# Optimization experiments

Hardware: AMD Instinct MI355X
Metric: run time of the kernel (lower is better)

The kernel has to match this reference:

```python
import jax, jax.numpy as jnp
import numpy as np

B, LC, LQ, D, F = 16, 2048, 256, 768, 768
MASK_VALUE = -1.0e12


def setup_inputs() -> dict:
    key = jax.random.key(0)
    ks = jax.random.split(key, 6)
    scale = 1.0 / np.sqrt(D)
    return {
        "x_cont": jax.random.normal(ks[0], (B, LC, D), dtype=jnp.float32),
        "x_ques": jax.random.normal(ks[1], (B, LQ, D), dtype=jnp.float32),
        "ques_len": jax.random.randint(ks[2], (B, 1), 0, LQ, dtype=jnp.int32),
        "WC": jax.random.normal(ks[3], (D, F), dtype=jnp.float32) * scale,
        "WQ": jax.random.normal(ks[4], (D, F), dtype=jnp.float32) * scale,
        "V": jax.random.normal(ks[5], (2 * D, F), dtype=jnp.float32) * scale,
    }


def _mask_logits(logits, ques_len):
    # Original: one_hot(ques_len[:,0], Lq) -> 1 - cumsum along Lq -> tile over Lc.
    # mask[b, j] = 1 if j < ques_len[b] else 0.
    lq = logits.shape[-1]
    oh = jax.nn.one_hot(ques_len[:, 0], lq, dtype=jnp.float32)  # [B, Lq]
    valid = 1.0 - jnp.cumsum(oh, axis=1)                         # [B, Lq]
    return logits + MASK_VALUE * (1.0 - valid)[:, None, :]       # broadcast over Lc


def reference(x_cont, x_ques, ques_len, WC, WQ, V):
    filters = WC.shape[-1]
    x_cont_ = jax.nn.relu(jnp.einsum("bcd,df->bcf", x_cont, WC))  # [B, Lc, F]
    x_ques_ = jax.nn.relu(jnp.einsum("bqd,df->bqf", x_ques, WQ))  # [B, Lq, F]
    logits = jnp.einsum("bcf,bqf->bcq", x_cont_, x_ques_) / jnp.sqrt(
        jnp.asarray(filters, dtype=x_cont.dtype)
    )  # [B, Lc, Lq]
    logits = _mask_logits(logits, ques_len)
    attn = jax.nn.softmax(logits, axis=-1)
    C = jnp.einsum("bcq,bqd->bcd", attn, x_ques)                  # [B, Lc, D]
    res = jnp.concatenate([x_cont, C], axis=2)                    # [B, Lc, 2D]
    gate = jax.nn.sigmoid(jnp.einsum("bce,ef->bcf", res, V))      # [B, Lc, F]
    return gate
```

## Files before the change

kernel.cpp:

```cpp
#include <hip/hip_runtime.h>
#include <hip/hip_bf16.h>
#include <cstdint>


using bf16 = __hip_bfloat16;
typedef __attribute__((ext_vector_type(8))) __bf16 bf16x8;
typedef __attribute__((ext_vector_type(4))) float f32x4;

typedef __attribute__((address_space(1))) const uint32_t GU32;
typedef __attribute__((address_space(3))) uint32_t LU32;

__device__ __forceinline__ void gll16(const bf16* g, bf16* l) {
  __builtin_amdgcn_global_load_lds((GU32*)g, (LU32*)l, 16, 0, 0);
}
__device__ __forceinline__ f32x4 mfma_bf16(bf16x8 a, bf16x8 b, f32x4 c) {
  return __builtin_amdgcn_mfma_f32_16x16x32_bf16(a, b, c, 0, 0, 0);
}
__device__ __forceinline__ bf16x8 ld_frag(const bf16* p) {
  return *reinterpret_cast<const bf16x8*>(p);
}
__device__ __forceinline__ int swz(int r) { return (r & 3) ^ ((r >> 2) & 1); }

__device__ __forceinline__ unsigned short f2bf_bits(float x) {
  bf16 b = __float2bfloat16(x);
  union { bf16 b; unsigned short s; } u;
  u.b = b;
  return u.s;
}

__global__ __launch_bounds__(256) void prep(
    const float* __restrict__ WC, const float* __restrict__ WQ,
    const float* __restrict__ V, const float* __restrict__ x_cont,
    const float* __restrict__ x_ques,
    bf16* __restrict__ Wct, bf16* __restrict__ Wqt,
    bf16* __restrict__ xcB, bf16* __restrict__ xqB) {
  const int bid = blockIdx.x;
  const int tid = threadIdx.x;
  if (bid < 2304) {
    __shared__ float tile[32][33];
    const int z = bid / 576, t = bid % 576;
    const float* in = (z == 0) ? WC : (z == 1) ? WQ : (z == 2) ? V : V + (long)768 * 768;
    bf16* out = (z == 0) ? Wct : (z == 1) ? Wqt
              : (z == 2) ? Wct + (long)768 * 768 : Wqt + (long)768 * 768;
    const int c0 = (t % 24) * 32, r0 = (t / 24) * 32;
    const int tx = tid & 31, ty = tid >> 5;
#pragma unroll
    for (int i = ty; i < 32; i += 8)
      tile[i][tx] = in[(long)(r0 + i) * 768 + (c0 + tx)];
    __syncthreads();
#pragma unroll
    for (int i = ty; i < 32; i += 8)
      out[(long)(c0 + i) * 768 + (r0 + tx)] = __float2bfloat16(tile[tx][i]);
  } else if (bid < 5376) {
    long i = (long)(bid - 2304) * 256 + tid;
#pragma unroll
    for (int k = 0; k < 8; ++k, i += 786432) {
      float4 v = reinterpret_cast<const float4*>(x_cont)[i];
      ushort4 o;
      o.x = f2bf_bits(v.x); o.y = f2bf_bits(v.y);
      o.z = f2bf_bits(v.z); o.w = f2bf_bits(v.w);
      reinterpret_cast<ushort4*>(xcB)[i] = o;
    }
  } else {
    long i = (long)(bid - 5376) * 256 + tid;
#pragma unroll
    for (int k = 0; k < 4; ++k, i += 196608) {
      float4 v = reinterpret_cast<const float4*>(x_ques)[i];
      ushort4 o;
      o.x = f2bf_bits(v.x); o.y = f2bf_bits(v.y);
      o.z = f2bf_bits(v.z); o.w = f2bf_bits(v.w);
      reinterpret_cast<ushort4*>(xqB)[i] = o;
    }
  }
}

__global__ __launch_bounds__(256) void gemm_bt_split(
    const bf16* __restrict__ A, long lda,
    const bf16* __restrict__ Bt, long ldb,
    bf16* __restrict__ O1, bf16* __restrict__ O2t, int K) {
  __shared__ __align__(16) bf16 As[128 * 32];
  __shared__ __align__(16) bf16 Bs[128 * 32];
  const int tid = threadIdx.x;
  const int wave = tid >> 6;
  const int lane = tid & 63;
  const int l16 = lane & 15;
  const int kh = lane >> 4;
  const int wm = (wave >> 1) * 64;
  const int wn = (wave & 1) * 64;
  const long row0 = (long)blockIdx.x * 128;
  const long col0 = (long)blockIdx.y * 128;
  const int srow = tid >> 2;
  const int scol = ((tid & 3) ^ swz(srow)) * 8;

  const bf16* ap0 = A + (row0 + srow) * lda + scol;
  const bf16* ap1 = ap0 + 64 * lda;
  const bf16* bp0 = Bt + (col0 + srow) * ldb + scol;
  const bf16* bp1 = bp0 + 64 * ldb;
  bf16* as0 = As + wave * 512;
  bf16* as1 = as0 + 2048;
  bf16* bs0 = Bs + wave * 512;
  bf16* bs1 = bs0 + 2048;

  const int xc = (kh ^ swz(l16)) * 8;
  f32x4 acc[4][4] = {};

  for (int k0 = 0; k0 < K; k0 += 32) {
    gll16(ap0 + k0, as0);
    gll16(ap1 + k0, as1);
    gll16(bp0 + k0, bs0);
    gll16(bp1 + k0, bs1);
    __syncthreads();
    bf16x8 af[4], bfr[4];
#pragma unroll
    for (int i = 0; i < 4; ++i)
      af[i] = ld_frag(As + (wm + i * 16 + l16) * 32 + xc);
#pragma unroll
    for (int j = 0; j < 4; ++j)
      bfr[j] = ld_frag(Bs + (wn + j * 16 + l16) * 32 + xc);
#pragma unroll
    for (int i = 0; i < 4; ++i)
#pragma unroll
      for (int j = 0; j < 4; ++j)
        acc[i][j] = mfma_bf16(af[i], bfr[j], acc[i][j]);
    __syncthreads();
  }

  const bool isO1 = col0 < 768;
#pragma unroll
  for (int i = 0; i < 4; ++i)
#pragma unroll
    for (int j = 0; j < 4; ++j) {
      const long rowb = row0 + wm + i * 16 + kh * 4;
      const long col = col0 + wn + j * 16 + l16;
      if (isO1) {
#pragma unroll
        for (int r = 0; r < 4; ++r)
          O1[(rowb + r) * 768 + col] = __float2bfloat16(fmaxf(acc[i][j][r], 0.0f));
      } else {
        const int d = (int)(col - 768);
        const int b2 = (int)(rowb >> 8);
        const int q = (int)(rowb & 255);
        ushort4 u;
        u.x = f2bf_bits(acc[i][j][0]);
        u.y = f2bf_bits(acc[i][j][1]);
        u.z = f2bf_bits(acc[i][j][2]);
        u.w = f2bf_bits(acc[i][j][3]);
        *reinterpret_cast<ushort4*>(O2t + ((long)b2 * 768 + d) * 256 + q) = u;
      }
    }
}

__global__ __launch_bounds__(512, 2) void gemm4b(
    const bf16* __restrict__ A, long lda,
    const bf16* __restrict__ Bt, long ldb,
    bf16* __restrict__ O1, bf16* __restrict__ O2, int K) {
  extern __shared__ __align__(16) bf16 smem[];
  const int tid = threadIdx.x;
  const int wid = tid >> 6;
  const int lane = tid & 63;
  const int l15 = lane & 15;
  const int g = lane >> 4;
  const int wm = wid >> 2;
  const int wn = wid & 3;

  const int lin = blockIdx.x;
  const int per = (int)gridDim.x >> 3;
  const int wgid = (lin & 7) * per + (lin >> 3);
  const long row0 = (long)(wgid / 6) * 256;
  const long col0 = (long)(wgid % 6) * 256;

  const int srow = lane >> 2;
  const int sc = ((lane & 3) ^ swz(srow)) * 8;
  const int w16 = wid * 16;
  const bf16* Ab = A + (row0 + srow) * lda + sc;
  const bf16* Bb = Bt + (col0 + srow) * ldb + sc;

  f32x4 acc[8][4] = {};

  auto stageA = [&](int buf, int kk) {
    bf16* d = smem + buf * 16384 + w16 * 32;
    gll16(Ab + (long)w16 * lda + kk, d);
    gll16(Ab + (long)(128 + w16) * lda + kk, d + 128 * 32);
  };
  auto stageB = [&](int buf, int kk) {
    bf16* d = smem + buf * 16384 + 8192 + w16 * 32;
    gll16(Bb + (long)w16 * ldb + kk, d);
    gll16(Bb + (long)(128 + w16) * ldb + kk, d + 128 * 32);
  };
  const int xc = (g ^ swz(l15)) * 8;
  auto ldA = [&](int buf, int m) {
    int row = wm * 128 + m * 16 + l15;
    return ld_frag(smem + buf * 16384 + row * 32 + xc);
  };
  auto ldB = [&](int buf, int n) {
    int row = wn * 64 + n * 16 + l15;
    return ld_frag(smem + buf * 16384 + 8192 + row * 32 + xc);
  };

  stageA(0, 0);
  stageB(0, 0);
  stageA(1, 32);
  stageB(1, 32);
  stageA(2, 64);
  stageB(2, 64);

  const int NT = K >> 5;
  bf16x8 av[4], bv[4];

  for (int t = 0; t < NT; ++t) {
    const int cur = t & 3;

    if (t <= NT - 3)
      asm volatile("s_waitcnt vmcnt(8)\n\ts_barrier" ::: "memory");
    else if (t == NT - 2)
      asm volatile("s_waitcnt vmcnt(4)\n\ts_barrier" ::: "memory");
    else
      asm volatile("s_waitcnt vmcnt(0)\n\ts_barrier" ::: "memory");

    if (t + 3 < NT) {
      stageA((t + 3) & 3, (t + 3) << 5);
      stageB((t + 3) & 3, (t + 3) << 5);
    }

#pragma unroll
    for (int n = 0; n < 4; ++n) bv[n] = ldB(cur, n);
#pragma unroll
    for (int m = 0; m < 4; ++m) av[m] = ldA(cur, m);
    __builtin_amdgcn_s_setprio(1);
#pragma unroll
    for (int m = 0; m < 4; ++m)
#pragma unroll
      for (int n = 0; n < 4; ++n) acc[m][n] = mfma_bf16(av[m], bv[n], acc[m][n]);
    __builtin_amdgcn_s_setprio(0);

#pragma unroll
    for (int m = 0; m < 4; ++m) av[m] = ldA(cur, 4 + m);
    __builtin_amdgcn_s_setprio(1);
#pragma unroll
    for (int m = 0; m < 4; ++m)
#pragma unroll
      for (int n = 0; n < 4; ++n)
        acc[4 + m][n] = mfma_bf16(av[m], bv[n], acc[4 + m][n]);
    __builtin_amdgcn_s_setprio(0);
  }

  const bool isO1 = col0 < 768;
#pragma unroll
  for (int m = 0; m < 8; ++m)
#pragma unroll
    for (int n = 0; n < 4; ++n)
#pragma unroll
      for (int r = 0; r < 4; ++r) {
        long row = row0 + wm * 128 + m * 16 + g * 4 + r;
        long col = col0 + wn * 64 + n * 16 + l15;
        float v = acc[m][n][r];
        if (isO1)
          O1[row * 768 + col] = __float2bfloat16(fmaxf(v, 0.0f));
        else
          O2[row * 768 + (col - 768)] = __float2bfloat16(v);
      }
}

__global__ __launch_bounds__(512) void attn3(
    const bf16* __restrict__ xcW, const bf16* __restrict__ xqW,
    const bf16* __restrict__ xqVT, const bf16* __restrict__ G1,
    const int* __restrict__ qlen_arr, float* __restrict__ out) {
  extern __shared__ __align__(16) bf16 smem[];
  bf16* P = smem;
  float* wred = (float*)(smem + 49152);
  float* wsum = wred + 512;

  const int lin = blockIdx.x;
  const int xcd = lin & 7;
  const int jj = lin >> 3;
  const int b = xcd * 2 + (jj >> 4);
  const int ct = jj & 15;

  const int tid = threadIdx.x;
  const int wid = tid >> 6;
  const int lane = tid & 63;
  const int l16 = lane & 15;
  const int kh = lane >> 4;
  const int wm = wid >> 2;
  const int wn = wid & 3;

  const long crow0 = (long)b * 2048 + (long)ct * 128;
  const int srow = lane >> 2;
  const int sc = ((lane & 3) ^ swz(srow)) * 8;
  const int xcr = (kh ^ swz(l16)) * 8;

  const bf16* ap = xcW + (crow0 + wid * 16 + srow) * 768 + sc;
  const bf16* bp = xqW + ((long)b * 256 + wid * 32 + srow) * 768 + sc;
  const bf16* bp2 = bp + 16 * 768;

  auto stage = [&](int buf, int k0) {
    gll16(ap + k0, smem + buf * 12288 + wid * 512);
    bf16* bd = smem + buf * 12288 + 4096 + wid * 1024;
    gll16(bp + k0, bd);
    gll16(bp2 + k0, bd + 512);
  };

  f32x4 acc[4][4] = {};
  stage(0, 0);
  stage(1, 32);
  stage(2, 64);

  for (int t = 0; t < 24; ++t) {
    const int cur = t & 3;

    if (t <= 21)
      asm volatile("s_waitcnt vmcnt(6)\n\ts_barrier" ::: "memory");
    else if (t == 22)
      asm volatile("s_waitcnt vmcnt(3)\n\ts_barrier" ::: "memory");
    else
      asm volatile("s_waitcnt vmcnt(0)\n\ts_barrier" ::: "memory");

    if (t + 3 < 24) stage((t + 3) & 3, (t + 3) * 32);

    const bf16* Ac = smem + cur * 12288;
    const bf16* Bc = Ac + 4096;
    bf16x8 af[4], bfr[4];
#pragma unroll
    for (int i = 0; i < 4; ++i)
      af[i] = ld_frag(Ac + (wm * 64 + i * 16 + l16) * 32 + xcr);
#pragma unroll
    for (int j = 0; j < 4; ++j)
      bfr[j] = ld_frag(Bc + (wn * 64 + j * 16 + l16) * 32 + xcr);
    __builtin_amdgcn_s_setprio(1);
#pragma unroll
    for (int i = 0; i < 4; ++i)
#pragma unroll
      for (int j = 0; j < 4; ++j)
        acc[i][j] = mfma_bf16(af[i], bfr[j], acc[i][j]);
    __builtin_amdgcn_s_setprio(0);
  }

  const float scale = 0.036084391824351615f;
  const int qlen = qlen_arr[b];

#pragma unroll
  for (int i = 0; i < 4; ++i)
#pragma unroll
    for (int j = 0; j < 4; ++j) {
      int col = wn * 64 + j * 16 + l16;
      float m = (col >= qlen) ? -1.0e12f : 0.0f;
#pragma unroll
      for (int r = 0; r < 4; ++r)
        acc[i][j][r] = acc[i][j][r] * scale + m;
    }

#pragma unroll
  for (int i = 0; i < 4; ++i)
#pragma unroll
    for (int r = 0; r < 4; ++r) {
      float mx = fmaxf(fmaxf(acc[i][0][r], acc[i][1][r]),
                       fmaxf(acc[i][2][r], acc[i][3][r]));
      mx = fmaxf(mx, __shfl_xor(mx, 1));
      mx = fmaxf(mx, __shfl_xor(mx, 2));
      mx = fmaxf(mx, __shfl_xor(mx, 4));
      mx = fmaxf(mx, __shfl_xor(mx, 8));
      if (l16 == 0) wred[(wm * 64 + i * 16 + kh * 4 + r) * 4 + wn] = mx;
    }
  __syncthreads();

#pragma unroll
  for (int i = 0; i < 4; ++i)
#pragma unroll
    for (int r = 0; r < 4; ++r) {
      int row = wm * 64 + i * 16 + kh * 4 + r;
      float gm = fmaxf(fmaxf(wred[row * 4 + 0], wred[row * 4 + 1]),
                       fmaxf(wred[row * 4 + 2], wred[row * 4 + 3]));
      float s = 0.0f;
#pragma unroll
      for (int j = 0; j < 4; ++j) {
        float e = __expf(acc[i][j][r] - gm);
        acc[i][j][r] = e;
        s += e;
      }
      s += __shfl_xor(s, 1);
      s += __shfl_xor(s, 2);
      s += __shfl_xor(s, 4);
      s += __shfl_xor(s, 8);
      if (l16 == 0) wsum[row * 4 + wn] = s;
    }
  __syncthreads();

#pragma unroll
  for (int i = 0; i < 4; ++i)
#pragma unroll
    for (int r = 0; r < 4; ++r) {
      int row = wm * 64 + i * 16 + kh * 4 + r;
      float inv = 1.0f / (wsum[row * 4 + 0] + wsum[row * 4 + 1] +
                          wsum[row * 4 + 2] + wsum[row * 4 + 3]);
#pragma unroll
      for (int j = 0; j < 4; ++j)
        P[row * 264 + wn * 64 + j * 16 + l16] = __float2bfloat16(acc[i][j][r] * inv);
    }
  __syncthreads();

  bf16x8 pf[4][8];
#pragma unroll
  for (int i = 0; i < 4; ++i)
#pragma unroll
    for (int kk = 0; kk < 8; ++kk)
      pf[i][kk] = ld_frag(P + (wm * 64 + i * 16 + l16) * 264 + kk * 32 + kh * 8);

  for (int nb = 0; nb < 3; ++nb) {
    const int n0 = nb * 256 + wn * 64;
    const bf16* btp = xqVT + ((long)b * 768 + n0) * 256;

    bf16 g1b[4][4][4];
#pragma unroll
    for (int i = 0; i < 4; ++i)
#pragma unroll
      for (int r = 0; r < 4; ++r) {
        long row = crow0 + wm * 64 + i * 16 + kh * 4 + r;
#pragma unroll
        for (int j = 0; j < 4; ++j)
          g1b[i][j][r] = G1[row * 768 + n0 + j * 16 + l16];
      }

    f32x4 a2[4][4] = {};
#pragma unroll
    for (int kk = 0; kk < 8; ++kk) {
      bf16x8 vf[4];
#pragma unroll
      for (int j = 0; j < 4; ++j)
        vf[j] = ld_frag(btp + (j * 16 + l16) * 256 + kk * 32 + kh * 8);
#pragma unroll
      for (int i = 0; i < 4; ++i)
#pragma unroll
        for (int j = 0; j < 4; ++j)
          a2[i][j] = mfma_bf16(pf[i][kk], vf[j], a2[i][j]);
    }
#pragma unroll
    for (int i = 0; i < 4; ++i)
#pragma unroll
      for (int j = 0; j < 4; ++j)
#pragma unroll
        for (int r = 0; r < 4; ++r) {
          long row = crow0 + wm * 64 + i * 16 + kh * 4 + r;
          int col = n0 + j * 16 + l16;
          float v = a2[i][j][r] + __bfloat162float(g1b[i][j][r]);
          out[row * 768 + col] = 1.0f / (1.0f + __expf(-v));
        }
  }
}

extern "C" void kernel_launch(void* const* d_in, const int* in_sizes, int n_in,
                              void* d_out, int out_size, void* d_ws, size_t ws_size,
                              hipStream_t stream) {
  const float* x_cont = (const float*)d_in[0];
  const float* x_ques = (const float*)d_in[1];
  const int* ques_len = (const int*)d_in[2];
  const float* WC = (const float*)d_in[3];
  const float* WQ = (const float*)d_in[4];
  const float* V = (const float*)d_in[5];
  float* out = (float*)d_out;

  bf16* Wct = (bf16*)d_ws;
  bf16* Wqt = Wct + (long)1536 * 768;
  bf16* xcB = Wqt + (long)1536 * 768;
  bf16* xqB = xcB + (long)32768 * 768;
  bf16* xcW = xqB + (long)4096 * 768;
  bf16* xqW = xcW + (long)32768 * 768;
  bf16* xqVT = xqW + (long)4096 * 768;
  bf16* G1 = xqVT + (long)16 * 768 * 256;

  (void)hipFuncSetAttribute(reinterpret_cast<const void*>(&gemm4b),
                            hipFuncAttributeMaxDynamicSharedMemorySize, 131072);
  (void)hipFuncSetAttribute(reinterpret_cast<const void*>(&attn3),
                            hipFuncAttributeMaxDynamicSharedMemorySize, 102400);

  prep<<<6144, 256, 0, stream>>>(WC, WQ, V, x_cont, x_ques, Wct, Wqt, xcB, xqB);

  gemm_bt_split<<<dim3(32, 12), 256, 0, stream>>>(xqB, 768, Wqt, 768, xqW, xqVT, 768);

  gemm4b<<<768, 512, 131072, stream>>>(xcB, 768, Wct, 768, xcW, G1, 768);

  attn3<<<256, 512, 102400, stream>>>(xcW, xqW, xqVT, G1, ques_len, out);
}
```

Baseline: 229.7 us.

## Split fused attention kernel into QK-softmax and PV-gate kernels via global P

Splits the fused attention kernel in two. The first kernel computes the masked softmax probabilities and writes them as bf16 to a global buffer that reuses the xcB workspace. The second kernel, launched on 1024 blocks of 256 threads, does P·(xq V) plus the G1 add and sigmoid. The aim is more parallelism in the memory-heavy output stage, which before ran on only 256 blocks. The cost is an extra global round trip for P (about 16 MB written and read) and one more kernel launch.

```diff
diff --git a/kernel.cpp b/kernel.cpp
--- a/kernel.cpp
+++ b/kernel.cpp
@@ -261,12 +261,10 @@
       }
 }
 
-__global__ __launch_bounds__(512) void attn3(
+__global__ __launch_bounds__(512) void attn_qk(
     const bf16* __restrict__ xcW, const bf16* __restrict__ xqW,
-    const bf16* __restrict__ xqVT, const bf16* __restrict__ G1,
-    const int* __restrict__ qlen_arr, float* __restrict__ out) {
+    const int* __restrict__ qlen_arr, bf16* __restrict__ Pg) {
   extern __shared__ __align__(16) bf16 smem[];
-  bf16* P = smem;
   float* wred = (float*)(smem + 49152);
   float* wsum = wred + 512;
 
@@ -394,57 +392,63 @@
                           wsum[row * 4 + 2] + wsum[row * 4 + 3]);
 #pragma unroll
       for (int j = 0; j < 4; ++j)
-        P[row * 264 + wn * 64 + j * 16 + l16] = __float2bfloat16(acc[i][j][r] * inv);
-    }
-  __syncthreads();
-
-  bf16x8 pf[4][8];
-#pragma unroll
-  for (int i = 0; i < 4; ++i)
+        Pg[(crow0 + row) * 256 + wn * 64 + j * 16 + l16] =
+            __float2bfloat16(acc[i][j][r] * inv);
+    }
+}
+
+__global__ __launch_bounds__(256) void attn_pv(
+    const bf16* __restrict__ Pg, const bf16* __restrict__ xqVT,
+    const bf16* __restrict__ G1, float* __restrict__ out) {
+  const int lin = blockIdx.x;
+  const int xcd = lin & 7;
+  const int j7 = lin >> 3;
+  const int b = xcd * 2 + (j7 >> 6);
+  const int ct = j7 & 63;
+
+  const int tid = threadIdx.x;
+  const int wn = tid >> 6;
+  const int lane = tid & 63;
+  const int l16 = lane & 15;
+  const int kh = lane >> 4;
+
+  const long row0 = (long)b * 2048 + (long)ct * 32;
+  const bf16* prow = Pg + row0 * 256;
+
+  bf16x8 pf[2][8];
+#pragma unroll
+  for (int m = 0; m < 2; ++m)
 #pragma unroll
     for (int kk = 0; kk < 8; ++kk)
-      pf[i][kk] = ld_frag(P + (wm * 64 + i * 16 + l16) * 264 + kk * 32 + kh * 8);
-
-  for (int nb = 0; nb < 3; ++nb) {
-    const int n0 = nb * 256 + wn * 64;
-    const bf16* btp = xqVT + ((long)b * 768 + n0) * 256;
-
-    bf16 g1b[4][4][4];
-#pragma unroll
-    for (int i = 0; i < 4; ++i)
+      pf[m][kk] = ld_frag(prow + (m * 16 + l16) * 256 + kk * 32 + kh * 8);
+
+  const bf16* vb = xqVT + ((long)b * 768 + wn * 192 + l16) * 256;
+  f32x4 acc[2][12] = {};
+
+#pragma unroll
+  for (int kk = 0; kk < 8; ++kk) {
+    bf16x8 vf[12];
+#pragma unroll
+    for (int j = 0; j < 12; ++j)
+      vf[j] = ld_frag(vb + (long)j * 16 * 256 + kk * 32 + kh * 8);
+#pragma unroll
+    for (int m = 0; m < 2; ++m)
+#pragma unroll
+      for (int j = 0; j < 12; ++j)
+        acc[m][j] = mfma_bf16(pf[m][kk], vf[j], acc[m][j]);
+  }
+
+#pragma unroll
+  for (int m = 0; m < 2; ++m)
+#pragma unroll
+    for (int j = 0; j < 12; ++j)
 #pragma unroll
       for (int r = 0; r < 4; ++r) {
-        long row = crow0 + wm * 64 + i * 16 + kh * 4 + r;
-#pragma unroll
-        for (int j = 0; j < 4; ++j)
-          g1b[i][j][r] = G1[row * 768 + n0 + j * 16 + l16];
+        long row = row0 + m * 16 + kh * 4 + r;
+        int col = wn * 192 + j * 16 + l16;
+        float v = acc[m][j][r] + __bfloat162float(G1[row * 768 + col]);
+        out[row * 768 + col] = 1.0f / (1.0f + __expf(-v));
       }
-
-    f32x4 a2[4][4] = {};
-#pragma unroll
-    for (int kk = 0; kk < 8; ++kk) {
-      bf16x8 vf[4];
-#pragma unroll
-      for (int j = 0; j < 4; ++j)
-        vf[j] = ld_frag(btp + (j * 16 + l16) * 256 + kk * 32 + kh * 8);
-#pragma unroll
-      for (int i = 0; i < 4; ++i)
-#pragma unroll
-        for (int j = 0; j < 4; ++j)
-          a2[i][j] = mfma_bf16(pf[i][kk], vf[j], a2[i][j]);
-    }
-#pragma unroll
-    for (int i = 0; i < 4; ++i)
-#pragma unroll
-      for (int j = 0; j < 4; ++j)
-#pragma unroll
-        for (int r = 0; r < 4; ++r) {
-          long row = crow0 + wm * 64 + i * 16 + kh * 4 + r;
-          int col = n0 + j * 16 + l16;
-          float v = a2[i][j][r] + __bfloat162float(g1b[i][j][r]);
-          out[row * 768 + col] = 1.0f / (1.0f + __expf(-v));
-        }
-  }
 }
 
 extern "C" void kernel_launch(void* const* d_in, const int* in_sizes, int n_in,
@@ -466,10 +470,11 @@
   bf16* xqW = xcW + (long)32768 * 768;
   bf16* xqVT = xqW + (long)4096 * 768;
   bf16* G1 = xqVT + (long)16 * 768 * 256;
+  bf16* Pg = xcB;
 
   (void)hipFuncSetAttribute(reinterpret_cast<const void*>(&gemm4b),
                             hipFuncAttributeMaxDynamicSharedMemorySize, 131072);
-  (void)hipFuncSetAttribute(reinterpret_cast<const void*>(&attn3),
+  (void)hipFuncSetAttribute(reinterpret_cast<const void*>(&attn_qk),
                             hipFuncAttributeMaxDynamicSharedMemorySize, 102400);
 
   prep<<<6144, 256, 0, stream>>>(WC, WQ, V, x_cont, x_ques, Wct, Wqt, xcB, xqB);
@@ -478,5 +483,7 @@
 
   gemm4b<<<768, 512, 131072, stream>>>(xcB, 768, Wct, 768, xcW, G1, 768);
 
-  attn3<<<256, 512, 102400, stream>>>(xcW, xqW, xqVT, G1, ques_len, out);
-}
+  attn_qk<<<256, 512, 102400, stream>>>(xcW, xqW, ques_len, Pg);
+
+  attn_pv<<<1024, 256, 0, stream>>>(Pg, xqVT, G1, out);
+}
```

New measurement: 263.3 us. 1.15x slower.
